# Kernel tuning notes

Hardware: AMD Instinct MI355X
Metric: run time of the kernel (lower is better)

## Reference

```python
import jax, jax.numpy as jnp
import numpy as np

B, T, C = 2, 2048, 1024
H = 16
HD = C // H  # head_dim = 64


def setup_inputs() -> dict:
    key = jax.random.key(0)
    ks = jax.random.split(key, 5)
    s = 0.02
    return {
        "x": jax.random.normal(ks[0], (B, T, C), dtype=jnp.float32),
        "Wqkv": jax.random.normal(ks[1], (C, 3 * C), dtype=jnp.float32) * s,
        "bqkv": jax.random.normal(ks[2], (3 * C,), dtype=jnp.float32) * s,
        "Wproj": jax.random.normal(ks[3], (C, C), dtype=jnp.float32) * s,
        "bproj": jax.random.normal(ks[4], (C,), dtype=jnp.float32) * s,
    }


def reference(x, Wqkv, bqkv, Wproj, bproj):
    b, t, c = x.shape
    qkv = x @ Wqkv + bqkv  # [B,T,3C]
    q, k, v = jnp.split(qkv, 3, axis=-1)
    # [B,T,C] -> [B,H,T,HD]
    q = q.reshape(b, t, H, HD).transpose(0, 2, 1, 3)
    k = k.reshape(b, t, H, HD).transpose(0, 2, 1, 3)
    v = v.reshape(b, t, H, HD).transpose(0, 2, 1, 3)
    scale = 1.0 / jnp.sqrt(jnp.float32(HD))
    att = jnp.einsum('bhqd,bhkd->bhqk', q, k) * scale  # [B,H,T,T]
    causal = jnp.tril(jnp.ones((t, t), dtype=bool))
    att = jnp.where(causal[None, None], att, jnp.float32(-jnp.inf))
    att = jax.nn.softmax(att, axis=-1)
    y = jnp.einsum('bhqk,bhkd->bhqd', att, v)  # [B,H,T,HD]
    y = y.transpose(0, 2, 1, 3).reshape(b, t, c)
    return y @ Wproj + bproj
```

## Files before the change

### kernel.cpp

```cpp
#include <hip/hip_runtime.h>

typedef unsigned short u16;
typedef __attribute__((ext_vector_type(4))) float f32x4;
typedef __attribute__((ext_vector_type(8))) short short8;

#define AS1 __attribute__((address_space(1)))
#define AS3 __attribute__((address_space(3)))

#define B_  2
#define T_  2048
#define C_  1024
#define H_  16
#define HD_ 64
#define N3C 3072
#define BT_ 4096

__device__ __forceinline__ u16 f2bf(float x) {
    unsigned u = __float_as_uint(x);
    u += 0x7fff + ((u >> 16) & 1);
    return (u16)(u >> 16);
}

__device__ __forceinline__ unsigned cvt_pk_bf16(float a, float b) {
    unsigned r;
    asm("v_cvt_pk_bf16_f32 %0, %1, %2" : "=v"(r) : "v"(a), "v"(b));
    return r;
}

__global__ __launch_bounds__(256)
void conv_all(const float* __restrict__ x, u16* __restrict__ xb,
              const float* __restrict__ Wq, u16* __restrict__ WqT,
              const float* __restrict__ Wp, u16* __restrict__ WpT) {
    __shared__ float tile[64][68];
    const int tid = threadIdx.x;
    const int b = blockIdx.x;
    if (b < 4096) {
        int i = b * 256 + tid;
        float4 f = ((const float4*)x)[i];
        uint2 o;
        o.x = cvt_pk_bf16(f.x, f.y);
        o.y = cvt_pk_bf16(f.z, f.w);
        ((uint2*)xb)[i] = o;
        return;
    }
    const float* W; u16* WT; int N, k0, n0;
    if (b < 4096 + 768) {
        int bb = b - 4096; W = Wq; WT = WqT; N = N3C;
        n0 = (bb % 48) * 64; k0 = (bb / 48) * 64;
    } else {
        int bb = b - 4864; W = Wp; WT = WpT; N = C_;
        n0 = (bb % 16) * 64; k0 = (bb / 16) * 64;
    }
    #pragma unroll
    for (int i = 0; i < 4; ++i) {
        int slot = tid + i * 256;
        int row = slot >> 4, c4 = (slot & 15) * 4;
        *(float4*)&tile[row][c4] = *(const float4*)&W[(size_t)(k0 + row) * N + n0 + c4];
    }
    __syncthreads();
    #pragma unroll
    for (int i = 0; i < 4; ++i) {
        int slot = tid + i * 256;
        int nn = slot >> 4, k4 = (slot & 15) * 4;
        uint2 o;
        o.x = cvt_pk_bf16(tile[k4 + 0][nn], tile[k4 + 1][nn]);
        o.y = cvt_pk_bf16(tile[k4 + 2][nn], tile[k4 + 3][nn]);
        *(uint2*)&WT[(size_t)(n0 + nn) * 1024 + k0 + k4] = o;
    }
}

__global__ __launch_bounds__(512, 2)
void qkv_gemm(const u16* __restrict__ A, const u16* __restrict__ BT,
              const float* __restrict__ bias,
              u16* __restrict__ q, u16* __restrict__ k, u16* __restrict__ vT) {
    __shared__ __align__(16) u16 As[4][256 * 32];
    __shared__ __align__(16) u16 Bs[4][256 * 32];
    const int tid  = threadIdx.x;
    const int lane = tid & 63, w = tid >> 6;
    const int wr = w >> 2, wc = w & 3;
    const int l15 = lane & 15, quad = lane >> 4;

    const int bid = blockIdx.x;
    const int bm = ((bid & 7) << 1) | ((bid >> 3) & 1);
    const int bn = bid >> 4;
    const int m0 = bm * 256, n0 = bn * 256;

    const int srow4 = lane >> 2;
    const int gch   = ((lane & 3) ^ ((lane >> 2) & 3) ^ (lane >> 4)) * 8;
    const int fl    = (l15 & 3) ^ (l15 >> 2);

    const u16* gA = A  + (size_t)(m0 + w * 16 + srow4) * 1024 + gch;
    const u16* gB = BT + (size_t)(n0 + w * 16 + srow4) * 1024 + gch;

    auto stageA = [&](int t) {
        const int sl = t & 3;
        #pragma unroll
        for (int j = 0; j < 2; ++j)
            __builtin_amdgcn_global_load_lds(
                (const AS1 void*)(gA + (size_t)j * 128 * 1024 + t * 32),
                (AS3 void*)(&As[sl][(j * 128 + w * 16) * 32]), 16, 0, 0);
    };
    auto stageB = [&](int t) {
        const int sl = t & 3;
        #pragma unroll
        for (int j = 0; j < 2; ++j)
            __builtin_amdgcn_global_load_lds(
                (const AS1 void*)(gB + (size_t)j * 128 * 1024 + t * 32),
                (AS3 void*)(&Bs[sl][(j * 128 + w * 16) * 32]), 16, 0, 0);
    };

    f32x4 acc[8][4] = {};

    stageA(0); stageB(0); stageA(1); stageB(1); stageA(2); stageB(2);
    asm volatile("s_waitcnt vmcnt(8)\n\ts_barrier" ::: "memory");

    const int aoff = (wr * 128 + l15) * 32 + (quad ^ fl) * 8;
    const int boff = (wc * 64  + l15) * 32 + (quad ^ fl) * 8;

    auto tile_body = [&](int t, bool doStage) {
        const u16* Ac = &As[t & 3][0];
        const u16* Bc = &Bs[t & 3][0];
        short8 a[8], b[4];
        #pragma unroll
        for (int mf = 0; mf < 4; ++mf)
            a[mf] = *(const short8*)&Ac[aoff + mf * 512];
        #pragma unroll
        for (int nf = 0; nf < 4; ++nf)
            b[nf] = *(const short8*)&Bc[boff + nf * 512];
        if (doStage) stageA(t + 3);
        asm volatile("s_barrier\n\ts_waitcnt lgkmcnt(0)" ::: "memory");
        __builtin_amdgcn_s_setprio(1);
        #pragma unroll
        for (int mf = 0; mf < 4; ++mf)
            #pragma unroll
            for (int nf = 0; nf < 4; ++nf)
                acc[mf][nf] = __builtin_amdgcn_mfma_f32_16x16x32_bf16(a[mf], b[nf], acc[mf][nf], 0, 0, 0);
        __builtin_amdgcn_s_setprio(0);
        asm volatile("s_barrier" ::: "memory");
        #pragma unroll
        for (int mf = 0; mf < 4; ++mf)
            a[4 + mf] = *(const short8*)&Ac[aoff + (4 + mf) * 512];
        if (doStage) stageB(t + 3);
        asm volatile("s_barrier\n\ts_waitcnt lgkmcnt(0)" ::: "memory");
        __builtin_amdgcn_s_setprio(1);
        #pragma unroll
        for (int mf = 0; mf < 4; ++mf)
            #pragma unroll
            for (int nf = 0; nf < 4; ++nf)
                acc[4 + mf][nf] = __builtin_amdgcn_mfma_f32_16x16x32_bf16(a[4 + mf], b[nf], acc[4 + mf][nf], 0, 0, 0);
        __builtin_amdgcn_s_setprio(0);
    };

    #pragma unroll 1
    for (int t = 0; t < 29; ++t) {
        tile_body(t, true);
        asm volatile("s_waitcnt vmcnt(8)\n\ts_barrier" ::: "memory");
    }
    tile_body(29, false);
    asm volatile("s_waitcnt vmcnt(4)\n\ts_barrier" ::: "memory");
    tile_body(30, false);
    asm volatile("s_waitcnt vmcnt(0)\n\ts_barrier" ::: "memory");
    tile_body(31, false);

    const int which = n0 >> 10;
    const float QSCALE = 0.125f * 1.4426950408889634f;
    #pragma unroll
    for (int nf = 0; nf < 4; ++nf) {
        const int n = n0 + wc * 64 + nf * 16 + l15;
        const int nl = n & 1023, h = nl >> 6, d = nl & 63;
        const float bv = bias[n];
        #pragma unroll
        for (int mf = 0; mf < 8; ++mf) {
            const int mb = m0 + wr * 128 + mf * 16 + quad * 4;
            const int bb = mb >> 11, t0 = mb & 2047;
            f32x4 v4 = acc[mf][nf];
            if (which == 0) {
                size_t base = ((size_t)(bb * H_ + h) * T_ + t0) * HD_ + d;
                #pragma unroll
                for (int r = 0; r < 4; ++r)
                    q[base + (size_t)r * HD_] = f2bf((v4[r] + bv) * QSCALE);
            } else if (which == 1) {
                size_t base = ((size_t)(bb * H_ + h) * T_ + t0) * HD_ + d;
                #pragma unroll
                for (int r = 0; r < 4; ++r)
                    k[base + (size_t)r * HD_] = f2bf(v4[r] + bv);
            } else {
                uint2 o;
                o.x = cvt_pk_bf16(v4[0] + bv, v4[1] + bv);
                o.y = cvt_pk_bf16(v4[2] + bv, v4[3] + bv);
                *(uint2*)&vT[((size_t)(bb * H_ + h) * HD_ + d) * T_ + t0] = o;
            }
        }
    }
}

__global__ __launch_bounds__(256, 4)
void attn(const u16* __restrict__ q, const u16* __restrict__ k,
          const u16* __restrict__ vT, u16* __restrict__ y) {
    __shared__ __align__(16) u16 Ks[2 * 64 * 64];
    __shared__ __align__(16) u16 Vs[2 * 64 * 64];
    const int tid = threadIdx.x;
    const int lane = tid & 63, w = tid >> 6;
    const int l15 = lane & 15, quad = lane >> 4;
    const int srow = lane >> 3, schunk = (lane & 7) ^ srow;
    const int idx = blockIdx.x;
    const int bh = idx & 31;
    const int qt = 31 - (idx >> 5);
    const u16* qp = q  + (size_t)bh * T_ * HD_;
    const u16* kp = k  + (size_t)bh * T_ * HD_;
    const u16* vp = vT + (size_t)bh * HD_ * T_;

    const int qrow = qt * 64 + w * 16 + l15;
    short8 qf[2];
    #pragma unroll
    for (int s = 0; s < 2; ++s)
        qf[s] = *(const short8*)&qp[(size_t)qrow * HD_ + s * 32 + quad * 8];

    auto stage = [&](int buf, int kt) {
        const int kb = kt * 64;
        asm volatile("s_waitcnt lgkmcnt(0)" ::: "memory");
        #pragma unroll
        for (int j = 0; j < 2; ++j) {
            int row = w * 16 + j * 8 + srow;
            __builtin_amdgcn_global_load_lds(
                (const AS1 void*)(kp + (size_t)(kb + row) * HD_ + schunk * 8),
                (AS3 void*)(Ks + buf * (64 * 64) + (w * 16 + j * 8) * 64), 16, 0, 0);
            __builtin_amdgcn_global_load_lds(
                (const AS1 void*)(vp + (size_t)row * T_ + kb + schunk * 8),
                (AS3 void*)(Vs + buf * (64 * 64) + (w * 16 + j * 8) * 64), 16, 0, 0);
        }
    };

    f32x4 o[4] = {};
    float l = 0.f;
    stage(0, 0);

    for (int kt = 0; kt <= qt; ++kt) {
        const int kb = kt * 64;
        const int cur = kt & 1;
        if (kt < qt) {
            stage(cur ^ 1, kt + 1);
            asm volatile("s_waitcnt vmcnt(4)\n\ts_barrier" ::: "memory");
        } else {
            asm volatile("s_waitcnt vmcnt(0)\n\ts_barrier" ::: "memory");
        }
        u16* Kc = Ks + cur * (64 * 64);
        const u16* Vc = Vs + cur * (64 * 64);

        short8 ka[4][2], va[4][2];
        #pragma unroll
        for (int ct = 0; ct < 4; ++ct)
            #pragma unroll
            for (int s = 0; s < 2; ++s) {
                int xo = ((s * 4 + quad) ^ (l15 & 7)) * 8;
                ka[ct][s] = *(const short8*)&Kc[(ct * 16 + l15) * 64 + xo];
                va[ct][s] = *(const short8*)&Vc[(ct * 16 + l15) * 64 + xo];
            }
        asm volatile("s_waitcnt lgkmcnt(0)\n\ts_barrier" ::: "memory");

        f32x4 st[4] = {};
        #pragma unroll
        for (int s = 0; s < 2; ++s)
            #pragma unroll
            for (int ct = 0; ct < 4; ++ct)
                st[ct] = __builtin_amdgcn_mfma_f32_16x16x32_bf16(ka[ct][s], qf[s], st[ct], 0, 0, 0);

        float pe[16];
        #pragma unroll
        for (int ct = 0; ct < 4; ++ct)
            #pragma unroll
            for (int r = 0; r < 4; ++r)
                pe[ct * 4 + r] = exp2f(st[ct][r]);
        if (kt == qt) {
            #pragma unroll
            for (int ct = 0; ct < 4; ++ct)
                #pragma unroll
                for (int r = 0; r < 4; ++r)
                    if ((kb + ct * 16 + quad * 4 + r) > qrow) pe[ct * 4 + r] = 0.f;
        }
        float psum = 0.f;
        #pragma unroll
        for (int i = 0; i < 16; ++i) psum += pe[i];
        l += psum;

        u16* Pw = Kc + (w * 16 + l15) * 64;
        #pragma unroll
        for (int ct = 0; ct < 4; ++ct) {
            int chunk = ct * 2 + (quad >> 1);
            int off = ((chunk ^ (l15 & 7)) << 3) + (quad & 1) * 4;
            uint2 pk;
            pk.x = cvt_pk_bf16(pe[ct * 4 + 0], pe[ct * 4 + 1]);
            pk.y = cvt_pk_bf16(pe[ct * 4 + 2], pe[ct * 4 + 3]);
            *(uint2*)&Pw[off] = pk;
        }
        asm volatile("s_waitcnt lgkmcnt(0)" ::: "memory");

        #pragma unroll
        for (int s = 0; s < 2; ++s) {
            short8 pb = *(const short8*)&Pw[(((s * 4 + quad) ^ (l15 & 7)) << 3)];
            #pragma unroll
            for (int n = 0; n < 4; ++n)
                o[n] = __builtin_amdgcn_mfma_f32_16x16x32_bf16(va[n][s], pb, o[n], 0, 0, 0);
        }
    }

    l += __shfl_xor(l, 16); l += __shfl_xor(l, 32);
    const float inv = 1.f / l;
    const int bb = bh >> 4, h = bh & 15;
    #pragma unroll
    for (int n = 0; n < 4; ++n) {
        uint2 pk;
        pk.x = cvt_pk_bf16(o[n][0] * inv, o[n][1] * inv);
        pk.y = cvt_pk_bf16(o[n][2] * inv, o[n][3] * inv);
        *(uint2*)&y[((size_t)(bb * T_ + qrow)) * C_ + h * 64 + n * 16 + quad * 4] = pk;
    }
}

__global__ __launch_bounds__(256, 3)
void proj_gemm(const u16* __restrict__ A, const u16* __restrict__ BT,
               const float* __restrict__ bias, float* __restrict__ out) {
    __shared__ __align__(16) u16 As[2 * 128 * 64];
    __shared__ __align__(16) u16 Bs[2 * 64 * 64];
    const int m0 = blockIdx.y * 128, n0 = blockIdx.x * 64;
    const int tid = threadIdx.x;
    const int lane = tid & 63, w = tid >> 6;
    const int l15 = lane & 15, quad = lane >> 4;
    const int row0 = (w & 1) * 64, col0 = (w >> 1) * 32;
    const int srow = lane >> 3;
    const int schunk = (lane & 7) ^ srow;
    f32x4 acc[4][2] = {};

    auto stage = [&](int buf, int k0) {
        #pragma unroll
        for (int j = 0; j < 4; ++j) {
            int rbase = w * 32 + j * 8;
            const u16* ga = A + (size_t)(m0 + rbase + srow) * 1024 + k0 + schunk * 8;
            __builtin_amdgcn_global_load_lds((const AS1 void*)ga,
                (AS3 void*)(As + buf * (128 * 64) + rbase * 64), 16, 0, 0);
        }
        #pragma unroll
        for (int j = 0; j < 2; ++j) {
            int rbase = w * 16 + j * 8;
            const u16* gb = BT + (size_t)(n0 + rbase + srow) * 1024 + k0 + schunk * 8;
            __builtin_amdgcn_global_load_lds((const AS1 void*)gb,
                (AS3 void*)(Bs + buf * (64 * 64) + rbase * 64), 16, 0, 0);
        }
    };

    stage(0, 0);
    #pragma unroll
    for (int it = 0; it < 16; ++it) {
        const int cur = it & 1;
        if (it + 1 < 16) {
            stage(cur ^ 1, (it + 1) * 64);
            asm volatile("s_waitcnt vmcnt(6)\n\ts_barrier" ::: "memory");
        } else {
            asm volatile("s_waitcnt vmcnt(0)\n\ts_barrier" ::: "memory");
        }
        const u16* Ac = As + cur * (128 * 64);
        const u16* Bc = Bs + cur * (64 * 64);
        #pragma unroll
        for (int s = 0; s < 2; ++s) {
            short8 a[4], b[2];
            #pragma unroll
            for (int rt = 0; rt < 4; ++rt) {
                int row = row0 + rt * 16 + l15;
                a[rt] = *(const short8*)&Ac[row * 64 + (((s * 4 + quad) ^ (l15 & 7)) * 8)];
            }
            #pragma unroll
            for (int ct = 0; ct < 2; ++ct) {
                int row = col0 + ct * 16 + l15;
                b[ct] = *(const short8*)&Bc[row * 64 + (((s * 4 + quad) ^ (l15 & 7)) * 8)];
            }
            #pragma unroll
            for (int rt = 0; rt < 4; ++rt)
                #pragma unroll
                for (int ct = 0; ct < 2; ++ct)
                    acc[rt][ct] = __builtin_amdgcn_mfma_f32_16x16x32_bf16(a[rt], b[ct], acc[rt][ct], 0, 0, 0);
        }
        asm volatile("s_waitcnt lgkmcnt(0)\n\ts_barrier" ::: "memory");
    }

    #pragma unroll
    for (int ct = 0; ct < 2; ++ct) {
        int n = n0 + col0 + ct * 16 + l15;
        float bv = bias[n];
        #pragma unroll
        for (int rt = 0; rt < 4; ++rt) {
            int mb = m0 + row0 + rt * 16 + quad * 4;
            f32x4 v4 = acc[rt][ct];
            #pragma unroll
            for (int r = 0; r < 4; ++r)
                out[(size_t)(mb + r) * 1024 + n] = v4[r] + bv;
        }
    }
}

extern "C" void kernel_launch(void* const* d_in, const int* in_sizes, int n_in,
                              void* d_out, int out_size, void* d_ws, size_t ws_size,
                              hipStream_t stream) {
    const float* x     = (const float*)d_in[0];
    const float* Wqkv  = (const float*)d_in[1];
    const float* bqkv  = (const float*)d_in[2];
    const float* Wproj = (const float*)d_in[3];
    const float* bproj = (const float*)d_in[4];

    u16* xb     = (u16*)d_ws;
    u16* WqkvT  = xb + (size_t)4 * 1024 * 1024;
    u16* WprojT = WqkvT + (size_t)3 * 1024 * 1024;
    u16* q      = WprojT + (size_t)1024 * 1024;
    u16* kk     = q + (size_t)4 * 1024 * 1024;
    u16* vT     = kk + (size_t)4 * 1024 * 1024;
    u16* y      = vT + (size_t)4 * 1024 * 1024;

    conv_all<<<5120, 256, 0, stream>>>(x, xb, Wqkv, WqkvT, Wproj, WprojT);
    qkv_gemm<<<192, 512, 0, stream>>>(xb, WqkvT, bqkv, q, kk, vT);
    attn<<<1024, 256, 0, stream>>>(q, kk, vT, y);
    proj_gemm<<<dim3(C_ / 64, BT_ / 128), 256, 0, stream>>>(y, WprojT, bproj, (float*)d_out);
}
```

Measured before the change: 188.3 us.

## Retile QKV GEMM to 256x192 blocks with K=64 double-buffered stages

Changes the QKV projection GEMM tile from 256x256 to 256x192 so the grid grows from 192 to 256 blocks, matching the CU count. K-step goes from 32 to 64 with double buffering in place of a four-deep ring, a new XOR swizzle over 8 chunks, and loads interleaved across four sub-phases per tile. Q/K/V selection is now done per column because a 192-wide tile can straddle the Q/K/V boundaries. The aim is to remove the wave-quantization tail, at the cost of a shallower prefetch pipeline and lower per-block arithmetic intensity.

Result: faster. 173.7 us (-7.8%).

```diff
diff --git a/kernel.cpp b/kernel.cpp
--- a/kernel.cpp
+++ b/kernel.cpp
@@ -73,100 +73,125 @@
 void qkv_gemm(const u16* __restrict__ A, const u16* __restrict__ BT,
               const float* __restrict__ bias,
               u16* __restrict__ q, u16* __restrict__ k, u16* __restrict__ vT) {
-    __shared__ __align__(16) u16 As[4][256 * 32];
-    __shared__ __align__(16) u16 Bs[4][256 * 32];
+    __shared__ __align__(16) u16 As[2][256 * 64];
+    __shared__ __align__(16) u16 Bs[2][192 * 64];
     const int tid  = threadIdx.x;
     const int lane = tid & 63, w = tid >> 6;
     const int wr = w >> 2, wc = w & 3;
     const int l15 = lane & 15, quad = lane >> 4;
+    const int srow = lane >> 3, schunk = (lane & 7) ^ srow;
 
     const int bid = blockIdx.x;
-    const int bm = ((bid & 7) << 1) | ((bid >> 3) & 1);
-    const int bn = bid >> 4;
-    const int m0 = bm * 256, n0 = bn * 256;
-
-    const int srow4 = lane >> 2;
-    const int gch   = ((lane & 3) ^ ((lane >> 2) & 3) ^ (lane >> 4)) * 8;
-    const int fl    = (l15 & 3) ^ (l15 >> 2);
-
-    const u16* gA = A  + (size_t)(m0 + w * 16 + srow4) * 1024 + gch;
-    const u16* gB = BT + (size_t)(n0 + w * 16 + srow4) * 1024 + gch;
-
-    auto stageA = [&](int t) {
-        const int sl = t & 3;
-        #pragma unroll
-        for (int j = 0; j < 2; ++j)
-            __builtin_amdgcn_global_load_lds(
-                (const AS1 void*)(gA + (size_t)j * 128 * 1024 + t * 32),
-                (AS3 void*)(&As[sl][(j * 128 + w * 16) * 32]), 16, 0, 0);
+    const int xcd = bid & 7, rr = bid >> 3;
+    const int bm = (xcd << 1) | (rr & 1);
+    const int bn = rr >> 1;
+    const int m0 = bm * 256, n0 = bn * 192;
+
+    const u16* gA = A  + (size_t)(m0 + w * 8  + srow) * 1024 + schunk * 8;
+    const u16* gB = BT + (size_t)(n0 + w * 24 + srow) * 1024 + schunk * 8;
+
+    auto stA = [&](int t, int qq) {
+        __builtin_amdgcn_global_load_lds(
+            (const AS1 void*)(gA + (size_t)qq * 64 * 1024 + t * 64),
+            (AS3 void*)(&As[t & 1][(w * 8 + qq * 64) * 64]), 16, 0, 0);
     };
-    auto stageB = [&](int t) {
-        const int sl = t & 3;
-        #pragma unroll
-        for (int j = 0; j < 2; ++j)
-            __builtin_amdgcn_global_load_lds(
-                (const AS1 void*)(gB + (size_t)j * 128 * 1024 + t * 32),
-                (AS3 void*)(&Bs[sl][(j * 128 + w * 16) * 32]), 16, 0, 0);
+    auto stB = [&](int t, int g) {
+        __builtin_amdgcn_global_load_lds(
+            (const AS1 void*)(gB + (size_t)g * 8 * 1024 + t * 64),
+            (AS3 void*)(&Bs[t & 1][(w * 24 + g * 8) * 64]), 16, 0, 0);
     };
 
-    f32x4 acc[8][4] = {};
-
-    stageA(0); stageB(0); stageA(1); stageB(1); stageA(2); stageB(2);
-    asm volatile("s_waitcnt vmcnt(8)\n\ts_barrier" ::: "memory");
-
-    const int aoff = (wr * 128 + l15) * 32 + (quad ^ fl) * 8;
-    const int boff = (wc * 64  + l15) * 32 + (quad ^ fl) * 8;
-
-    auto tile_body = [&](int t, bool doStage) {
-        const u16* Ac = &As[t & 3][0];
-        const u16* Bc = &Bs[t & 3][0];
-        short8 a[8], b[4];
-        #pragma unroll
-        for (int mf = 0; mf < 4; ++mf)
-            a[mf] = *(const short8*)&Ac[aoff + mf * 512];
-        #pragma unroll
-        for (int nf = 0; nf < 4; ++nf)
-            b[nf] = *(const short8*)&Bc[boff + nf * 512];
-        if (doStage) stageA(t + 3);
-        asm volatile("s_barrier\n\ts_waitcnt lgkmcnt(0)" ::: "memory");
-        __builtin_amdgcn_s_setprio(1);
-        #pragma unroll
-        for (int mf = 0; mf < 4; ++mf)
-            #pragma unroll
-            for (int nf = 0; nf < 4; ++nf)
-                acc[mf][nf] = __builtin_amdgcn_mfma_f32_16x16x32_bf16(a[mf], b[nf], acc[mf][nf], 0, 0, 0);
-        __builtin_amdgcn_s_setprio(0);
-        asm volatile("s_barrier" ::: "memory");
-        #pragma unroll
-        for (int mf = 0; mf < 4; ++mf)
-            a[4 + mf] = *(const short8*)&Ac[aoff + (4 + mf) * 512];
-        if (doStage) stageB(t + 3);
-        asm volatile("s_barrier\n\ts_waitcnt lgkmcnt(0)" ::: "memory");
-        __builtin_amdgcn_s_setprio(1);
-        #pragma unroll
-        for (int mf = 0; mf < 4; ++mf)
-            #pragma unroll
-            for (int nf = 0; nf < 4; ++nf)
-                acc[4 + mf][nf] = __builtin_amdgcn_mfma_f32_16x16x32_bf16(a[4 + mf], b[nf], acc[4 + mf][nf], 0, 0, 0);
-        __builtin_amdgcn_s_setprio(0);
-    };
+    f32x4 acc[8][3] = {};
+
+    stB(0, 0); stB(0, 1); stB(0, 2); stA(0, 0); stA(0, 2); stA(0, 1); stA(0, 3);
+    asm volatile("s_waitcnt vmcnt(2)\n\ts_barrier" ::: "memory");
 
     #pragma unroll 1
-    for (int t = 0; t < 29; ++t) {
-        tile_body(t, true);
-        asm volatile("s_waitcnt vmcnt(8)\n\ts_barrier" ::: "memory");
-    }
-    tile_body(29, false);
-    asm volatile("s_waitcnt vmcnt(4)\n\ts_barrier" ::: "memory");
-    tile_body(30, false);
-    asm volatile("s_waitcnt vmcnt(0)\n\ts_barrier" ::: "memory");
-    tile_body(31, false);
-
-    const int which = n0 >> 10;
+    for (int t = 0; t < 16; ++t) {
+        const u16* Ac = &As[t & 1][0];
+        const u16* Bc = &Bs[t & 1][0];
+        const bool st = (t < 15);
+        short8 a[4], b[3];
+
+        {
+            const int xo = (quad ^ (l15 & 7)) * 8;
+            #pragma unroll
+            for (int mf = 0; mf < 4; ++mf)
+                a[mf] = *(const short8*)&Ac[(wr * 128 + mf * 16 + l15) * 64 + xo];
+            #pragma unroll
+            for (int nf = 0; nf < 3; ++nf)
+                b[nf] = *(const short8*)&Bc[(wc * 48 + nf * 16 + l15) * 64 + xo];
+            if (st) { stB(t + 1, 0); stB(t + 1, 1); }
+            asm volatile("s_barrier\n\ts_waitcnt lgkmcnt(0)" ::: "memory");
+            __builtin_amdgcn_s_setprio(1);
+            #pragma unroll
+            for (int mf = 0; mf < 4; ++mf)
+                #pragma unroll
+                for (int nf = 0; nf < 3; ++nf)
+                    acc[mf][nf] = __builtin_amdgcn_mfma_f32_16x16x32_bf16(a[mf], b[nf], acc[mf][nf], 0, 0, 0);
+            __builtin_amdgcn_s_setprio(0);
+            if (st) asm volatile("s_waitcnt vmcnt(2)\n\ts_barrier" ::: "memory");
+            else    asm volatile("s_waitcnt vmcnt(0)\n\ts_barrier" ::: "memory");
+        }
+        {
+            const int xo = (quad ^ (l15 & 7)) * 8;
+            #pragma unroll
+            for (int mf = 0; mf < 4; ++mf)
+                a[mf] = *(const short8*)&Ac[(wr * 128 + (4 + mf) * 16 + l15) * 64 + xo];
+            if (st) { stB(t + 1, 2); stA(t + 1, 0); }
+            asm volatile("s_barrier\n\ts_waitcnt lgkmcnt(0)" ::: "memory");
+            __builtin_amdgcn_s_setprio(1);
+            #pragma unroll
+            for (int mf = 0; mf < 4; ++mf)
+                #pragma unroll
+                for (int nf = 0; nf < 3; ++nf)
+                    acc[4 + mf][nf] = __builtin_amdgcn_mfma_f32_16x16x32_bf16(a[mf], b[nf], acc[4 + mf][nf], 0, 0, 0);
+            __builtin_amdgcn_s_setprio(0);
+            asm volatile("s_barrier" ::: "memory");
+        }
+        {
+            const int xo = ((4 + quad) ^ (l15 & 7)) * 8;
+            #pragma unroll
+            for (int mf = 0; mf < 4; ++mf)
+                a[mf] = *(const short8*)&Ac[(wr * 128 + mf * 16 + l15) * 64 + xo];
+            #pragma unroll
+            for (int nf = 0; nf < 3; ++nf)
+                b[nf] = *(const short8*)&Bc[(wc * 48 + nf * 16 + l15) * 64 + xo];
+            if (st) stA(t + 1, 2);
+            asm volatile("s_barrier\n\ts_waitcnt lgkmcnt(0)" ::: "memory");
+            __builtin_amdgcn_s_setprio(1);
+            #pragma unroll
+            for (int mf = 0; mf < 4; ++mf)
+                #pragma unroll
+                for (int nf = 0; nf < 3; ++nf)
+                    acc[mf][nf] = __builtin_amdgcn_mfma_f32_16x16x32_bf16(a[mf], b[nf], acc[mf][nf], 0, 0, 0);
+            __builtin_amdgcn_s_setprio(0);
+            asm volatile("s_barrier" ::: "memory");
+        }
+        {
+            const int xo = ((4 + quad) ^ (l15 & 7)) * 8;
+            #pragma unroll
+            for (int mf = 0; mf < 4; ++mf)
+                a[mf] = *(const short8*)&Ac[(wr * 128 + (4 + mf) * 16 + l15) * 64 + xo];
+            if (st) { stA(t + 1, 1); stA(t + 1, 3); }
+            asm volatile("s_barrier\n\ts_waitcnt lgkmcnt(0)" ::: "memory");
+            __builtin_amdgcn_s_setprio(1);
+            #pragma unroll
+            for (int mf = 0; mf < 4; ++mf)
+                #pragma unroll
+                for (int nf = 0; nf < 3; ++nf)
+                    acc[4 + mf][nf] = __builtin_amdgcn_mfma_f32_16x16x32_bf16(a[mf], b[nf], acc[4 + mf][nf], 0, 0, 0);
+            __builtin_amdgcn_s_setprio(0);
+            if (st) asm volatile("s_waitcnt vmcnt(2)\n\ts_barrier" ::: "memory");
+            else    asm volatile("s_barrier" ::: "memory");
+        }
+    }
+
     const float QSCALE = 0.125f * 1.4426950408889634f;
     #pragma unroll
-    for (int nf = 0; nf < 4; ++nf) {
-        const int n = n0 + wc * 64 + nf * 16 + l15;
+    for (int nf = 0; nf < 3; ++nf) {
+        const int n = n0 + wc * 48 + nf * 16 + l15;
+        const int which = n >> 10;
         const int nl = n & 1023, h = nl >> 6, d = nl & 63;
         const float bv = bias[n];
         #pragma unroll
@@ -414,7 +439,7 @@
     u16* y      = vT + (size_t)4 * 1024 * 1024;
 
     conv_all<<<5120, 256, 0, stream>>>(x, xb, Wqkv, WqkvT, Wproj, WprojT);
-    qkv_gemm<<<192, 512, 0, stream>>>(xb, WqkvT, bqkv, q, kk, vT);
+    qkv_gemm<<<256, 512, 0, stream>>>(xb, WqkvT, bqkv, q, kk, vT);
     attn<<<1024, 256, 0, stream>>>(q, kk, vT, y);
     proj_gemm<<<dim3(C_ / 64, BT_ / 128), 256, 0, stream>>>(y, WprojT, bproj, (float*)d_out);
 }
```
